# Kernel tuning notes

Measured on AMD Instinct MI355X. Metric: run time of the kernel, lower is better.

## Reference

```python
import jax, jax.numpy as jnp
import numpy as np

B, N, DIM, H, DH = 8, 1024, 512, 8, 64
INNER = H * DH  # 512
G = DH // 4     # SE(3) groups of size 4 per head


def setup_inputs() -> dict:
    key = jax.random.key(0)
    ks = jax.random.split(key, 6)
    x = jax.random.normal(ks[0], (B, N, DIM), jnp.float32)
    rotations = jax.random.normal(ks[1], (B, N, 3, 3), jnp.float32)
    translations = jax.random.normal(ks[2], (B, N, 3), jnp.float32)
    # JaxLinear init: trunc-normal std = 1/sqrt(fan_in), zero bias
    w_qkv = jax.random.normal(ks[3], (DIM, 3 * INNER), jnp.float32) * (1.0 / np.sqrt(DIM))
    b_qkv = jnp.zeros((3 * INNER,), jnp.float32)
    w_out = jax.random.normal(ks[4], (INNER, DIM), jnp.float32) * (1.0 / np.sqrt(INNER))
    b_out = jnp.zeros((DIM,), jnp.float32)
    return {"x": x, "rotations": rotations, "translations": translations,
            "w_qkv": w_qkv, "b_qkv": b_qkv, "w_out": w_out, "b_out": b_out}


def _apply_pose(P, t, transpose):
    # P: [B,N,4,4]; t: [B,H,N,DH] -> reshape to groups of 4 and rotate each group
    tg = t.reshape(B, H, N, G, 4)
    sub = 'bnji,bhncj->bhnci' if transpose else 'bnij,bhncj->bhnci'
    return jnp.einsum(sub, P, tg).reshape(B, H, N, DH)


def reference(x, rotations, translations, w_qkv, b_qkv, w_out, b_out):
    scale = DH ** -0.5
    qkv = x @ w_qkv + b_qkv                      # [B,N,3*INNER]
    q, k, v = jnp.split(qkv, 3, axis=-1)
    to_heads = lambda t: t.reshape(B, N, H, DH).transpose(0, 2, 1, 3)  # b n (h d) -> b h n d
    q, k, v = to_heads(q), to_heads(k), to_heads(v)

    # SE(3) pose matrices
    eye4 = jnp.eye(4, dtype=x.dtype)
    Rt = jnp.swapaxes(rotations, -1, -2)
    t_inv = -jnp.einsum('bnij,bnj->bni', Rt, translations)
    P_qinv = (jnp.broadcast_to(eye4, (B, N, 4, 4))
              .at[..., :3, :3].set(Rt)
              .at[..., :3, 3].set(t_inv))       # inverted query poses
    P_kv = (jnp.broadcast_to(eye4, (B, N, 4, 4))
            .at[..., :3, :3].set(rotations)
            .at[..., :3, 3].set(translations))  # key/value poses

    # per-token rotation of q/k/v (q uses P_qinv^T per original einsum)
    q = _apply_pose(P_qinv, q, transpose=True)
    k = _apply_pose(P_kv, k, transpose=False)
    v = _apply_pose(P_kv, v, transpose=False)   # v_transform=True

    attn = jax.nn.softmax(jnp.einsum('bhqd,bhkd->bhqk', q, k) * scale, axis=-1)
    out = jnp.einsum('bhqk,bhkd->bhqd', attn, v)
    out = _apply_pose(P_qinv, out, transpose=False)  # inverse transform on output

    out = out.transpose(0, 2, 1, 3).reshape(B, N, INNER)  # b h n d -> b n (h d)
    return out @ w_out + b_out
```

## Files before the change

### kernel.cpp

```cpp
#include <hip/hip_runtime.h>
#include <math.h>

#define BSZ   8
#define NSEQ  1024
#define DIM   512
#define NH    8
#define DH    64
#define INNER 512
#define NTOK  (BSZ*NSEQ)
#define QKVN  (3*INNER)

typedef __bf16   bf16x8 __attribute__((ext_vector_type(8)));
typedef _Float16 f16x8  __attribute__((ext_vector_type(8)));
typedef float    f32x4  __attribute__((ext_vector_type(4)));
typedef unsigned u32x2  __attribute__((ext_vector_type(2)));

#define QSCL (0.125f * 1.44269504088896f)

static __device__ __forceinline__ ushort f2bf(float f) {
    union { float f; unsigned u; } v; v.f = f;
    unsigned r = (v.u + 0x7FFFu + ((v.u >> 16) & 1u)) >> 16;
    return (ushort)r;
}
static __device__ __forceinline__ ushort f2h(float f) {
    _Float16 h = (_Float16)f;
    return __builtin_bit_cast(unsigned short, h);
}
static __device__ __forceinline__ void async16(const void* g, void* l) {
    __builtin_amdgcn_global_load_lds(
        (const __attribute__((address_space(1))) unsigned int*)g,
        (__attribute__((address_space(3))) unsigned int*)l, 16, 0, 0);
}

__global__ __launch_bounds__(256) void prep_kernel(
    const float* __restrict__ x,  ushort* __restrict__ xf,
    const float* __restrict__ wq, ushort* __restrict__ wqT,
    const float* __restrict__ wo, ushort* __restrict__ woT)
{
    const int bid = blockIdx.x;
    if (bid < 4096) {
        const int i = bid*256 + threadIdx.x;
        float4 v = ((const float4*)x)[i];
        ushort4 h = { f2h(v.x), f2h(v.y), f2h(v.z), f2h(v.w) };
        ((ushort4*)xf)[i] = h;
        return;
    }
    __shared__ float tile[32][33];
    int K, F, bx, by; const float* in; ushort* outp; int is_q;
    if (bid < 4096 + 768) {
        const int id = bid - 4096;
        bx = id % 48; by = id / 48;
        K = DIM; F = QKVN; in = wq; outp = wqT; is_q = 1;
    } else {
        const int id = bid - 4864;
        bx = id % 16; by = id / 16;
        K = INNER; F = DIM; in = wo; outp = woT; is_q = 0;
    }
    const int lx = threadIdx.x & 31, ly = threadIdx.x >> 5;
#pragma unroll
    for (int u = 0; u < 4; u++) {
        const int k = by*32 + ly + u*8;
        tile[ly + u*8][lx] = in[(size_t)k*F + bx*32 + lx];
    }
    __syncthreads();
#pragma unroll
    for (int u = 0; u < 4; u++) {
        const int f = bx*32 + ly + u*8;
        const float v = tile[lx][ly + u*8];
        outp[(size_t)f*K + by*32 + lx] = is_q ? f2h(v) : f2bf(v);
    }
}

__global__ __launch_bounds__(256) void qkv_gemm_f16(
    const ushort* __restrict__ Ag,
    const ushort* __restrict__ Bg,
    const float* __restrict__ bias, const float* __restrict__ rot,
    const float* __restrict__ trans,
    ushort* __restrict__ qb, ushort* __restrict__ kb, ushort* __restrict__ vt)
{
    extern __shared__ __align__(16) char smem[];

    const int tid  = threadIdx.x;
    const int lane = tid & 63;
    const int w    = tid >> 6;
    const int c    = lane & 15;
    const int quad = lane >> 4;
    const int wr   = w >> 1, wc = w & 1;
    const int tn   = blockIdx.x;
    const int tf   = blockIdx.y;

    f32x4 acc[4][4] = {};

    const int part = w >> 1;
    const int g0   = (w & 1) * 4;
    const ushort* src = (part == 0) ? Ag : Bg;
    const ushort* wbase = src + (size_t)((part == 0 ? tf : tn)*128 + g0*16 + c)*DIM
                          + quad*8;

    auto stage = [&](int k0, int buf) {
#pragma unroll
        for (int g = 0; g < 4; g++)
            async16(wbase + (size_t)g*16*DIM + k0,
                    smem + buf*16384 + part*8192 + (g0 + g)*1024);
    };

    stage(0, 0);
    stage(32, 1);

    for (int ch = 0; ch < 16; ch++) {
        const int cur = ch % 3;
        if (ch < 15) {
            __asm__ volatile("s_waitcnt vmcnt(4)\n\ts_barrier" ::: "memory");
        } else {
            __asm__ volatile("s_waitcnt vmcnt(0)\n\ts_barrier" ::: "memory");
        }
        if (ch < 14) stage((ch+2)*32, (ch+2) % 3);

        const char* B = smem + cur*16384;
        f16x8 fa[4], fb[4];
#pragma unroll
        for (int i = 0; i < 4; i++)
            fa[i] = *(const f16x8*)(B + (wr*4 + i)*1024 + lane*16);
#pragma unroll
        for (int j = 0; j < 4; j++)
            fb[j] = *(const f16x8*)(B + 8192 + (wc*4 + j)*1024 + lane*16);
#pragma unroll
        for (int i = 0; i < 4; i++)
#pragma unroll
            for (int j = 0; j < 4; j++)
                acc[i][j] = __builtin_amdgcn_mfma_f32_16x16x32_f16(
                    fa[i], fb[j], acc[i][j], 0, 0, 0);
    }

    const int sec = tf >> 2;

#pragma unroll
    for (int j = 0; j < 4; j++) {
        const int tc = tn*128 + wc*64 + j*16 + c;
        const int bb = tc >> 10, n = tc & 1023;
        const float* R = rot   + (size_t)(bb*NSEQ + n)*9;
        const float* T = trans + (size_t)(bb*NSEQ + n)*3;
        const float R0=R[0],R1=R[1],R2=R[2],R3=R[3],R4=R[4],R5=R[5],R6=R[6],R7=R[7],R8=R[8];
        const float T0=T[0],T1=T[1],T2=T[2];
        float ti0 = 0.f, ti1 = 0.f, ti2 = 0.f;
        if (sec == 0) {
            ti0 = -(R0*T0 + R3*T1 + R6*T2);
            ti1 = -(R1*T0 + R4*T1 + R7*T2);
            ti2 = -(R2*T0 + R5*T1 + R8*T2);
        }
#pragma unroll
        for (int i = 0; i < 4; i++) {
            const int fr = tf*128 + wr*64 + i*16 + quad*4;
            const int fl = fr & 511;
            const int h  = fl >> 6, d = fl & 63;
            float4 bv = *(const float4*)(bias + fr);
            const float g0v = acc[i][j][0] + bv.x;
            const float g1v = acc[i][j][1] + bv.y;
            const float g2v = acc[i][j][2] + bv.z;
            const float g3v = acc[i][j][3] + bv.w;
            if (sec == 0) {
                float o0 = (R0*g0v + R1*g1v + R2*g2v) * QSCL;
                float o1 = (R3*g0v + R4*g1v + R5*g2v) * QSCL;
                float o2 = (R6*g0v + R7*g1v + R8*g2v) * QSCL;
                float o3 = (ti0*g0v + ti1*g1v + ti2*g2v + g3v) * QSCL;
                ushort4 ov = { f2bf(o0), f2bf(o1), f2bf(o2), f2bf(o3) };
                *(ushort4*)(qb + ((size_t)((bb*NH + h)*NSEQ + n))*DH + d) = ov;
            } else {
                float o0 = R0*g0v + R1*g1v + R2*g2v + T0*g3v;
                float o1 = R3*g0v + R4*g1v + R5*g2v + T1*g3v;
                float o2 = R6*g0v + R7*g1v + R8*g2v + T2*g3v;
                float o3 = g3v;
                if (sec == 1) {
                    ushort4 ov = { f2bf(o0), f2bf(o1), f2bf(o2), f2bf(o3) };
                    *(ushort4*)(kb + ((size_t)((bb*NH + h)*NSEQ + n))*DH + d) = ov;
                } else {
                    ushort* vtb = vt + ((size_t)(bb*NH + h)*DH + d)*NSEQ + n;
                    vtb[0*NSEQ] = f2bf(o0);
                    vtb[1*NSEQ] = f2bf(o1);
                    vtb[2*NSEQ] = f2bf(o2);
                    vtb[3*NSEQ] = f2bf(o3);
                }
            }
        }
    }
}

__global__ __launch_bounds__(256, 2) void attn_mfma_kernel(
    const ushort* __restrict__ qb, const ushort* __restrict__ kb,
    const ushort* __restrict__ vt, const float* __restrict__ rot,
    const float* __restrict__ trans, ushort* __restrict__ om)
{
    __shared__ __align__(16) char smem[58624];

    const int tid  = threadIdx.x;
    const int lane = tid & 63;
    const int w    = tid >> 6;
    const int c    = lane & 15;
    const int quad = lane >> 4;

    const int o   = blockIdx.x;
    const int wid = (o & 7) * 128 + (o >> 3);
    const int qt  = wid & 15;
    const int bh  = wid >> 4;
    const int bb = bh >> 3, h = bh & 7;

    const ushort* Q = qb + (size_t)bh * NSEQ * DH;
    const ushort* K = kb + (size_t)bh * NSEQ * DH;
    const ushort* V = vt + (size_t)bh * DH * NSEQ;

    bf16x8 qf[2];
    {
        const ushort* qrow = Q + (size_t)(qt*64 + w*16 + c)*DH + quad*8;
        qf[0] = *(const bf16x8*)(qrow);
        qf[1] = *(const bf16x8*)(qrow + 32);
    }

    f32x4 Oacc[4] = {};
    float lsum = 0.f;

    auto stage = [&](int kt, int buf) {
#pragma unroll
        for (int u = 0; u < 2; u++) {
            const int seg = w + u*4;
            const int nt = seg >> 1, hh = seg & 1;
            const ushort* g = K + (size_t)(kt*64 + nt*16 + c)*DH + hh*32 + quad*8;
            async16(g, smem + buf*16384 + seg*1024);
        }
#pragma unroll
        for (int u = 0; u < 2; u++) {
            const int s2 = w + u*4;
            const int nt = s2 >> 1, kc = s2 & 1;
            const ushort* g = V + (size_t)(nt*16 + c)*NSEQ + kt*64 + kc*32 + quad*8;
            async16(g, smem + buf*16384 + 8192 + s2*1024);
        }
    };

    stage(0, 0);
    stage(1, 1);

    ushort (*Psw)[72] = (ushort (*)[72])(smem + 49152 + w*2304);
    char*  Pb = smem + 49152 + w*2304 + c*144;
    float* lsumS = (float*)(smem + 58368);

    for (int kt = 0; kt < 16; kt++) {
        const int cur = kt % 3;
        if (kt < 15) {
            __asm__ volatile("s_waitcnt vmcnt(4)\n\ts_barrier" ::: "memory");
        } else {
            __asm__ volatile("s_waitcnt vmcnt(0)\n\ts_barrier" ::: "memory");
        }
        if (kt < 14) stage(kt + 2, (kt + 2) % 3);

        const char* Kb = smem + cur*16384;
        const char* Vb = smem + cur*16384 + 8192;

        f32x4 s[4];
#pragma unroll
        for (int nt = 0; nt < 4; nt++) {
            bf16x8 k0 = *(const bf16x8*)(Kb + (nt*2+0)*1024 + lane*16);
            bf16x8 k1 = *(const bf16x8*)(Kb + (nt*2+1)*1024 + lane*16);
            f32x4 a = {0.f, 0.f, 0.f, 0.f};
            a = __builtin_amdgcn_mfma_f32_16x16x32_bf16(k0, qf[0], a, 0, 0, 0);
            a = __builtin_amdgcn_mfma_f32_16x16x32_bf16(k1, qf[1], a, 0, 0, 0);
            s[nt] = a;
        }

#pragma unroll
        for (int nt = 0; nt < 4; nt++) {
            const float p0 = exp2f(s[nt][0]);
            const float p1 = exp2f(s[nt][1]);
            const float p2 = exp2f(s[nt][2]);
            const float p3 = exp2f(s[nt][3]);
            lsum += (p0 + p1) + (p2 + p3);
            unsigned w0, w1;
            __asm__("v_cvt_pk_bf16_f32 %0, %1, %2" : "=v"(w0) : "v"(p0), "v"(p1));
            __asm__("v_cvt_pk_bf16_f32 %0, %1, %2" : "=v"(w1) : "v"(p2), "v"(p3));
            u32x2 pk = {w0, w1};
            *(u32x2*)(Pb + nt*32 + quad*8) = pk;
        }
        __asm__ volatile("s_waitcnt lgkmcnt(0)" ::: "memory");

#pragma unroll
        for (int kc2 = 0; kc2 < 2; kc2++) {
            bf16x8 vfr[4];
#pragma unroll
            for (int nt = 0; nt < 4; nt++)
                vfr[nt] = *(const bf16x8*)(Vb + (nt*2+kc2)*1024 + lane*16);
            bf16x8 a = *(const bf16x8*)&Psw[c][kc2*32 + quad*8];
#pragma unroll
            for (int nt = 0; nt < 4; nt++)
                Oacc[nt] = __builtin_amdgcn_mfma_f32_16x16x32_bf16(
                    a, vfr[nt], Oacc[nt], 0, 0, 0);
        }
    }

    lsum += __shfl_xor(lsum, 16);
    lsum += __shfl_xor(lsum, 32);
    if (lane < 16) lsumS[w*16 + c] = lsum;

    __syncthreads();
    float (*Osh)[68] = (float (*)[68])smem;
#pragma unroll
    for (int nt = 0; nt < 4; nt++)
#pragma unroll
        for (int r = 0; r < 4; r++)
            Osh[w*16 + quad*4 + r][nt*16 + c] = Oacc[nt][r];
    __syncthreads();

#pragma unroll
    for (int u = 0; u < 4; u++) {
        const int t   = tid + u*256;
        const int row = t >> 4;
        const int g   = t & 15;
        const int n   = qt*64 + row;
        const float inv = 1.f / lsumS[row];
        const float o0 = Osh[row][g*4+0] * inv, o1 = Osh[row][g*4+1] * inv;
        const float o2 = Osh[row][g*4+2] * inv, o3 = Osh[row][g*4+3] * inv;
        const float* R = rot   + (size_t)(bb*NSEQ + n)*9;
        const float* T = trans + (size_t)(bb*NSEQ + n)*3;
        const float ti0 = -(R[0]*T[0] + R[3]*T[1] + R[6]*T[2]);
        const float ti1 = -(R[1]*T[0] + R[4]*T[1] + R[7]*T[2]);
        const float ti2 = -(R[2]*T[0] + R[5]*T[1] + R[8]*T[2]);
        const float p0 = R[0]*o0 + R[3]*o1 + R[6]*o2 + ti0*o3;
        const float p1 = R[1]*o0 + R[4]*o1 + R[7]*o2 + ti1*o3;
        const float p2 = R[2]*o0 + R[5]*o1 + R[8]*o2 + ti2*o3;
        const float p3 = o3;
        ushort4 hv = { f2bf(p0), f2bf(p1), f2bf(p2), f2bf(p3) };
        *(ushort4*)(om + (size_t)(bb*NSEQ + n)*INNER + h*DH + g*4) = hv;
    }
}

__global__ __launch_bounds__(256) void out_gemm_mfma(
    const ushort* __restrict__ Ag, const ushort* __restrict__ Bg,
    const float* __restrict__ bias, float* __restrict__ out)
{
    extern __shared__ __align__(16) char smem[];

    const int tid  = threadIdx.x;
    const int lane = tid & 63;
    const int w    = tid >> 6;
    const int c    = lane & 15;
    const int quad = lane >> 4;
    const int wr   = w >> 1, wc = w & 1;
    const int tn   = blockIdx.x;
    const int tf   = blockIdx.y;

    f32x4 acc[4][4] = {};

    const int part = w >> 1;
    const int g0   = (w & 1) * 4;
    const ushort* src = (part == 0) ? Ag : Bg;
    const ushort* wbase = src + (size_t)((part == 0 ? tf : tn)*128 + g0*16 + c)*INNER
                          + quad*8;

    auto stage = [&](int k0, int buf) {
#pragma unroll
        for (int g = 0; g < 4; g++)
            async16(wbase + (size_t)g*16*INNER + k0,
                    smem + buf*16384 + part*8192 + (g0 + g)*1024);
    };

    stage(0, 0);
    stage(32, 1);
    stage(64, 2);

    for (int ch = 0; ch < 16; ch++) {
        const int cur = ch & 3;
        if (ch < 14) {
            __asm__ volatile("s_waitcnt vmcnt(8)\n\ts_barrier" ::: "memory");
        } else if (ch == 14) {
            __asm__ volatile("s_waitcnt vmcnt(4)\n\ts_barrier" ::: "memory");
        } else {
            __asm__ volatile("s_waitcnt vmcnt(0)\n\ts_barrier" ::: "memory");
        }
        if (ch < 13) stage((ch+3)*32, (ch+3) & 3);

        const char* B = smem + cur*16384;
        bf16x8 fa[4], fb[4];
#pragma unroll
        for (int i = 0; i < 4; i++)
            fa[i] = *(const bf16x8*)(B + (wr*4 + i)*1024 + lane*16);
#pragma unroll
        for (int j = 0; j < 4; j++)
            fb[j] = *(const bf16x8*)(B + 8192 + (wc*4 + j)*1024 + lane*16);
#pragma unroll
        for (int i = 0; i < 4; i++)
#pragma unroll
            for (int j = 0; j < 4; j++)
                acc[i][j] = __builtin_amdgcn_mfma_f32_16x16x32_bf16(
                    fa[i], fb[j], acc[i][j], 0, 0, 0);
    }

#pragma unroll
    for (int j = 0; j < 4; j++) {
        const int tc = tn*128 + wc*64 + j*16 + c;
#pragma unroll
        for (int i = 0; i < 4; i++) {
            const int fr = tf*128 + wr*64 + i*16 + quad*4;
            float4 bv = *(const float4*)(bias + fr);
            float4 ov = { acc[i][j][0] + bv.x, acc[i][j][1] + bv.y,
                          acc[i][j][2] + bv.z, acc[i][j][3] + bv.w };
            *(float4*)(out + (size_t)tc*DIM + fr) = ov;
        }
    }
}

extern "C" void kernel_launch(void* const* d_in, const int* in_sizes, int n_in,
                              void* d_out, int out_size, void* d_ws, size_t ws_size,
                              hipStream_t stream) {
    (void)in_sizes; (void)n_in; (void)out_size; (void)ws_size;
    const float* x     = (const float*)d_in[0];
    const float* rot   = (const float*)d_in[1];
    const float* trans = (const float*)d_in[2];
    const float* w_qkv = (const float*)d_in[3];
    const float* b_qkv = (const float*)d_in[4];
    const float* w_out = (const float*)d_in[5];
    const float* b_out = (const float*)d_in[6];
    float* out = (float*)d_out;

    const size_t HB = (size_t)BSZ*NH*NSEQ*DH;
    ushort* qb   = (ushort*)d_ws;
    ushort* kb   = qb   + HB;
    ushort* vt   = kb   + HB;
    ushort* woTh = vt   + HB;
    ushort* wqTh = woTh + (size_t)DIM*INNER;
    ushort* xf   = wqTh + (size_t)QKVN*DIM;
    ushort* om   = xf;

    static int s_attr_done = 0;
    if (!s_attr_done) {
        (void)hipFuncSetAttribute((const void*)out_gemm_mfma,
            hipFuncAttributeMaxDynamicSharedMemorySize, 65536);
        s_attr_done = 1;
    }

    prep_kernel<<<dim3(5120), 256, 0, stream>>>(
        x, xf, w_qkv, wqTh, w_out, woTh);

    qkv_gemm_f16<<<dim3(NTOK/128, QKVN/128), 256, 49152, stream>>>(
        wqTh, xf, b_qkv, rot, trans, qb, kb, vt);
    attn_mfma_kernel<<<dim3(1024), 256, 0, stream>>>(
        qb, kb, vt, rot, trans, om);
    out_gemm_mfma<<<dim3(NTOK/128, DIM/128), 256, 65536, stream>>>(
        woTh, om, b_out, out);
}
```

Baseline: 167.2 us.

## Shuffle P through registers in attention and double-buffer QKV GEMM to cut LDS

The attention kernel no longer writes the softmax probabilities to LDS and reads them back. It repacks the bf16 P fragments into the MFMA A-operand layout with cross-lane shuffles, which shrinks shared memory and raises launch bounds to 3 blocks per CU. The QKV GEMM goes from a triple-buffered to a double-buffered LDS pipeline with an extra barrier per chunk, cutting dynamic shared memory from 48KB to 32KB to allow more resident blocks. The trade-offs are extra shuffle instructions, an extra barrier and a shallower prefetch depth.

After: 167.0 us. Within noise of the previous version (-0.1%).

```diff
diff --git a/kernel.cpp b/kernel.cpp
--- a/kernel.cpp
+++ b/kernel.cpp
@@ -13,7 +13,7 @@
 typedef __bf16   bf16x8 __attribute__((ext_vector_type(8)));
 typedef _Float16 f16x8  __attribute__((ext_vector_type(8)));
 typedef float    f32x4  __attribute__((ext_vector_type(4)));
-typedef unsigned u32x2  __attribute__((ext_vector_type(2)));
+typedef unsigned u32x4  __attribute__((ext_vector_type(4)));
 
 #define QSCL (0.125f * 1.44269504088896f)
 
@@ -105,16 +105,15 @@
     };
 
     stage(0, 0);
-    stage(32, 1);
 
     for (int ch = 0; ch < 16; ch++) {
-        const int cur = ch % 3;
+        const int cur = ch & 1, nxt = cur ^ 1;
         if (ch < 15) {
+            stage((ch+1)*32, nxt);
             __asm__ volatile("s_waitcnt vmcnt(4)\n\ts_barrier" ::: "memory");
         } else {
             __asm__ volatile("s_waitcnt vmcnt(0)\n\ts_barrier" ::: "memory");
         }
-        if (ch < 14) stage((ch+2)*32, (ch+2) % 3);
 
         const char* B = smem + cur*16384;
         f16x8 fa[4], fb[4];
@@ -130,6 +129,7 @@
             for (int j = 0; j < 4; j++)
                 acc[i][j] = __builtin_amdgcn_mfma_f32_16x16x32_f16(
                     fa[i], fb[j], acc[i][j], 0, 0, 0);
+        __asm__ volatile("s_waitcnt lgkmcnt(0)\n\ts_barrier" ::: "memory");
     }
 
     const int sec = tf >> 2;
@@ -185,12 +185,12 @@
     }
 }
 
-__global__ __launch_bounds__(256, 2) void attn_mfma_kernel(
+__global__ __launch_bounds__(256, 3) void attn_mfma_kernel(
     const ushort* __restrict__ qb, const ushort* __restrict__ kb,
     const ushort* __restrict__ vt, const float* __restrict__ rot,
     const float* __restrict__ trans, ushort* __restrict__ om)
 {
-    __shared__ __align__(16) char smem[58624];
+    __shared__ __align__(16) char smem[49408];
 
     const int tid  = threadIdx.x;
     const int lane = tid & 63;
@@ -238,9 +238,7 @@
     stage(0, 0);
     stage(1, 1);
 
-    ushort (*Psw)[72] = (ushort (*)[72])(smem + 49152 + w*2304);
-    char*  Pb = smem + 49152 + w*2304 + c*144;
-    float* lsumS = (float*)(smem + 58368);
+    float* lsumS = (float*)(smem + 49152);
 
     for (int kt = 0; kt < 16; kt++) {
         const int cur = kt % 3;
@@ -265,6 +263,7 @@
             s[nt] = a;
         }
 
+        unsigned lo[4], hi[4];
 #pragma unroll
         for (int nt = 0; nt < 4; nt++) {
             const float p0 = exp2f(s[nt][0]);
@@ -272,21 +271,28 @@
             const float p2 = exp2f(s[nt][2]);
             const float p3 = exp2f(s[nt][3]);
             lsum += (p0 + p1) + (p2 + p3);
-            unsigned w0, w1;
-            __asm__("v_cvt_pk_bf16_f32 %0, %1, %2" : "=v"(w0) : "v"(p0), "v"(p1));
-            __asm__("v_cvt_pk_bf16_f32 %0, %1, %2" : "=v"(w1) : "v"(p2), "v"(p3));
-            u32x2 pk = {w0, w1};
-            *(u32x2*)(Pb + nt*32 + quad*8) = pk;
-        }
-        __asm__ volatile("s_waitcnt lgkmcnt(0)" ::: "memory");
-
+            __asm__("v_cvt_pk_bf16_f32 %0, %1, %2" : "=v"(lo[nt]) : "v"(p0), "v"(p1));
+            __asm__("v_cvt_pk_bf16_f32 %0, %1, %2" : "=v"(hi[nt]) : "v"(p2), "v"(p3));
+        }
+
+        const int sA = (quad & 1) * 32 + c;
+        const int sB = sA + 16;
+        const bool hiq = (quad >> 1) != 0;
 #pragma unroll
         for (int kc2 = 0; kc2 < 2; kc2++) {
+            const int n0 = kc2*2, n1 = kc2*2 + 1;
+            unsigned a0 = __shfl(lo[n0], sA), b0 = __shfl(lo[n1], sA);
+            unsigned a1 = __shfl(hi[n0], sA), b1 = __shfl(hi[n1], sA);
+            unsigned a2 = __shfl(lo[n0], sB), b2 = __shfl(lo[n1], sB);
+            unsigned a3 = __shfl(hi[n0], sB), b3 = __shfl(hi[n1], sB);
+            u32x4 av = { hiq ? b0 : a0, hiq ? b1 : a1,
+                         hiq ? b2 : a2, hiq ? b3 : a3 };
+            bf16x8 a = __builtin_bit_cast(bf16x8, av);
+
             bf16x8 vfr[4];
 #pragma unroll
             for (int nt = 0; nt < 4; nt++)
                 vfr[nt] = *(const bf16x8*)(Vb + (nt*2+kc2)*1024 + lane*16);
-            bf16x8 a = *(const bf16x8*)&Psw[c][kc2*32 + quad*8];
 #pragma unroll
             for (int nt = 0; nt < 4; nt++)
                 Oacc[nt] = __builtin_amdgcn_mfma_f32_16x16x32_bf16(
@@ -437,7 +443,7 @@
     prep_kernel<<<dim3(5120), 256, 0, stream>>>(
         x, xf, w_qkv, wqTh, w_out, woTh);
 
-    qkv_gemm_f16<<<dim3(NTOK/128, QKVN/128), 256, 49152, stream>>>(
+    qkv_gemm_f16<<<dim3(NTOK/128, QKVN/128), 256, 32768, stream>>>(
         wqTh, xf, b_qkv, rot, trans, qb, kb, vt);
     attn_mfma_kernel<<<dim3(1024), 256, 0, stream>>>(
         qb, kb, vt, rot, trans, om);
```
